# Optimization experiments

Hardware: AMD Instinct MI355X
Metric: run time of the kernel (lower is better)

Reference implementation:

```python
import jax, jax.numpy as jnp
import numpy as np

B, S, IN, H, OUT, L = 64, 2048, 208, 100, 98, 2


def setup_inputs() -> dict:
    key = jax.random.key(0)
    ks = jax.random.split(key, 11)
    sc = 1.0 / np.sqrt(H)  # pytorch GRU init scale
    return {
        "sequence": jax.random.normal(ks[0], (B, S, IN), jnp.float32),
        "h0": jnp.zeros((L, B, H), jnp.float32),
        "w_ih_l0": jax.random.normal(ks[1], (3 * H, IN), jnp.float32) * sc,
        "w_hh_l0": jax.random.normal(ks[2], (3 * H, H), jnp.float32) * sc,
        "b_ih_l0": jax.random.normal(ks[3], (3 * H,), jnp.float32) * sc,
        "b_hh_l0": jax.random.normal(ks[4], (3 * H,), jnp.float32) * sc,
        "w_ih_l1": jax.random.normal(ks[5], (3 * H, H), jnp.float32) * sc,
        "w_hh_l1": jax.random.normal(ks[6], (3 * H, H), jnp.float32) * sc,
        "b_ih_l1": jax.random.normal(ks[7], (3 * H,), jnp.float32) * sc,
        "b_hh_l1": jax.random.normal(ks[8], (3 * H,), jnp.float32) * sc,
        "w_out": jax.random.normal(ks[9], (OUT, H), jnp.float32) * sc,
        "b_out": jax.random.normal(ks[10], (OUT,), jnp.float32) * sc,
    }


def _gru_layer(x, h0, w_ih, w_hh, b_ih, b_hh):
    # x: (B,S,Din), h0: (B,H). PyTorch GRU gate order: r, z, n.
    Hd = h0.shape[-1]
    xg = jnp.einsum("bsi,gi->bsg", x, w_ih) + b_ih  # (B,S,3H) input projections, batched GEMM

    def step(h, xg_t):
        hg = h @ w_hh.T + b_hh  # (B,3H)
        xr, xz, xn = xg_t[:, :Hd], xg_t[:, Hd:2 * Hd], xg_t[:, 2 * Hd:]
        hr, hz, hn = hg[:, :Hd], hg[:, Hd:2 * Hd], hg[:, 2 * Hd:]
        r = jax.nn.sigmoid(xr + hr)
        z = jax.nn.sigmoid(xz + hz)
        n = jnp.tanh(xn + r * hn)
        h_new = (1.0 - z) * n + z * h
        return h_new, h_new

    h_last, ys = jax.lax.scan(step, h0, jnp.swapaxes(xg, 0, 1))  # scan over time
    return jnp.swapaxes(ys, 0, 1), h_last  # (B,S,H)


def reference(sequence, h0, w_ih_l0, w_hh_l0, b_ih_l0, b_hh_l0,
              w_ih_l1, w_hh_l1, b_ih_l1, b_hh_l1, w_out, b_out):
    # 2-layer unidirectional GRU (eval mode: inter-layer dropout inactive) + linear head
    y0, _ = _gru_layer(sequence, h0[0], w_ih_l0, w_hh_l0, b_ih_l0, b_hh_l0)
    y1, _ = _gru_layer(y0, h0[1], w_ih_l1, w_hh_l1, b_ih_l1, b_hh_l1)
    return jnp.einsum("bsh,oh->bso", y1, w_out) + b_out  # (B,S,OUT)
```

## Files before the change

kernel.cpp:

```cpp
#include <hip/hip_runtime.h>
#include <hip/hip_bf16.h>


#define GB_BM 64
#define GB_BN 64
#define GB_BK 16

__global__ __launch_bounds__(256)
void gemm_bias(const float* __restrict__ A, const float* __restrict__ W,
               const float* __restrict__ bias, float* __restrict__ C,
               int Sc, long a_bs, long a_ss, long c_bs, long c_ss,
               int N, int K)
{
    __shared__ float As[GB_BK][68];
    __shared__ float Bs[GB_BK][68];
    const int tid = threadIdx.x;
    const int m0 = blockIdx.x * GB_BM;
    const int n0 = blockIdx.y * GB_BN;

    const int lm = tid >> 2;
    const int lk = (tid & 3) << 2;
    const int row = m0 + lm;
    const float* arow = A + (long)(row / Sc) * a_bs + (long)(row % Sc) * a_ss;
    const int wrow = n0 + lm;
    const float* wrp = W + (long)wrow * K;
    const bool wv_ok = (wrow < N);

    const int tx = tid & 15;
    const int ty = tid >> 4;

    float acc[4][4] = {};

    for (int k0 = 0; k0 < K; k0 += GB_BK) {
        float4 av, bv;
        if (k0 + GB_BK <= K) {
            av = *(const float4*)(arow + k0 + lk);
            bv = wv_ok ? *(const float4*)(wrp + k0 + lk) : make_float4(0.f,0.f,0.f,0.f);
        } else {
            av = make_float4(0.f,0.f,0.f,0.f);
            bv = make_float4(0.f,0.f,0.f,0.f);
            const int kb = k0 + lk;
            if (kb + 0 < K) { av.x = arow[kb+0]; if (wv_ok) bv.x = wrp[kb+0]; }
            if (kb + 1 < K) { av.y = arow[kb+1]; if (wv_ok) bv.y = wrp[kb+1]; }
            if (kb + 2 < K) { av.z = arow[kb+2]; if (wv_ok) bv.z = wrp[kb+2]; }
            if (kb + 3 < K) { av.w = arow[kb+3]; if (wv_ok) bv.w = wrp[kb+3]; }
        }
        As[lk+0][lm] = av.x; As[lk+1][lm] = av.y; As[lk+2][lm] = av.z; As[lk+3][lm] = av.w;
        Bs[lk+0][lm] = bv.x; Bs[lk+1][lm] = bv.y; Bs[lk+2][lm] = bv.z; Bs[lk+3][lm] = bv.w;
        __syncthreads();
        #pragma unroll
        for (int kk = 0; kk < GB_BK; kk++) {
            float4 a  = *(const float4*)&As[kk][ty << 2];
            float4 bb = *(const float4*)&Bs[kk][tx << 2];
            float ar[4] = {a.x, a.y, a.z, a.w};
            float br[4] = {bb.x, bb.y, bb.z, bb.w};
            #pragma unroll
            for (int i = 0; i < 4; i++)
                #pragma unroll
                for (int j = 0; j < 4; j++)
                    acc[i][j] += ar[i] * br[j];
        }
        __syncthreads();
    }

    #pragma unroll
    for (int i = 0; i < 4; i++) {
        const int r = m0 + (ty << 2) + i;
        float* crow = C + (long)(r / Sc) * c_bs + (long)(r % Sc) * c_ss;
        #pragma unroll
        for (int j = 0; j < 4; j++) {
            const int col = n0 + (tx << 2) + j;
            if (col < N) crow[col] = acc[i][j] + bias[col];
        }
    }
}


__device__ __forceinline__ float fsig(float x)  { return 1.f / (1.f + __expf(-x)); }
__device__ __forceinline__ float ftanh(float x) { return 1.f - 2.f / (1.f + __expf(2.f * x)); }

__global__ __launch_bounds__(640, 1)
void gru_scan(const float* __restrict__ xg, const float* __restrict__ w_hh,
              const float* __restrict__ b_hh, const float* __restrict__ h_init,
              float* __restrict__ h_state, float* __restrict__ y,
              int Sc, int first)
{
    __shared__ __align__(16) float hs[100];
    __shared__ float hg_lds[300];
    __shared__ float xg_lds[300];

    const int tid = threadIdx.x;
    const int b = blockIdx.x;
    const int half = tid & 1;
    const int g = tid >> 1;
    const bool dot = (tid < 600);
    const bool even = dot && (half == 0);

    float4 wv[13];
    float bhh = 0.f;
    if (dot) {
        const float* wb = w_hh + g * 100 + half * 48;
        #pragma unroll
        for (int i = 0; i < 13; i++) wv[i] = *(const float4*)(wb + 4 * i);
        if (!half) wv[12] = make_float4(0.f, 0.f, 0.f, 0.f);
    }
    if (even) bhh = b_hh[g];

    float hcur = 0.f;
    if (tid < 100) {
        hcur = first ? h_init[b * 100 + tid] : h_state[b * 100 + tid];
        hs[tid] = hcur;
    }

    const float* xgb = xg + (size_t)b * Sc * 300;
    float xnext = 0.f;
    if (even) xnext = xgb[g];
    __syncthreads();

    for (int t = 0; t < Sc; t++) {
        const float xcur = xnext;
        if (even && (t + 1 < Sc)) xnext = xgb[(size_t)(t + 1) * 300 + g];

        float tot = 0.f;
        if (dot) {
            const float4* hs4 = (const float4*)hs;
            const int base = half * 12;
            float a0 = 0.f, a1 = 0.f;
            #pragma unroll
            for (int i = 0; i < 13; i++) {
                const float4 h4 = hs4[base + i];
                const float4 w = wv[i];
                a0 += w.x * h4.x; a1 += w.y * h4.y;
                a0 += w.z * h4.z; a1 += w.w * h4.w;
            }
            tot = a0 + a1;
            tot += __shfl_down(tot, 1);
        }
        if (even) { hg_lds[g] = tot + bhh; xg_lds[g] = xcur; }
        __syncthreads();

        if (tid < 100) {
            const float xr = xg_lds[tid], xz = xg_lds[100 + tid], xn = xg_lds[200 + tid];
            const float hr = hg_lds[tid], hz = hg_lds[100 + tid], hn = hg_lds[200 + tid];
            const float r = fsig(xr + hr);
            const float z = fsig(xz + hz);
            const float n = ftanh(xn + r * hn);
            hcur = (1.f - z) * n + z * hcur;
            hs[tid] = hcur;
            y[((size_t)b * Sc + t) * 100 + tid] = hcur;
        }
        __syncthreads();
    }

    if (tid < 100) h_state[b * 100 + tid] = hcur;
}


extern "C" void kernel_launch(void* const* d_in, const int* in_sizes, int n_in,
                              void* d_out, int out_size, void* d_ws, size_t ws_size,
                              hipStream_t stream)
{
    const float* seq    = (const float*)d_in[0];
    const float* h0     = (const float*)d_in[1];
    const float* w_ih0  = (const float*)d_in[2];
    const float* w_hh0  = (const float*)d_in[3];
    const float* b_ih0  = (const float*)d_in[4];
    const float* b_hh0  = (const float*)d_in[5];
    const float* w_ih1  = (const float*)d_in[6];
    const float* w_hh1  = (const float*)d_in[7];
    const float* b_ih1  = (const float*)d_in[8];
    const float* b_hh1  = (const float*)d_in[9];
    const float* w_out  = (const float*)d_in[10];
    const float* b_out  = (const float*)d_in[11];
    float* out = (float*)d_out;

    const int B = 64, S = 2048, IN = 208, H = 100, G = 300, OUT = 98;

    int Sc = S;
    while (Sc > 16) {
        size_t need = ((size_t)B * Sc * (G + H + H) + 2 * (size_t)B * H) * sizeof(float);
        if (need <= ws_size) break;
        Sc >>= 1;
    }
    const int NC = S / Sc;

    float* h0s = (float*)d_ws;
    float* h1s = h0s + (size_t)B * H;
    float* y0c = h1s + (size_t)B * H;
    float* y1c = y0c + (size_t)B * Sc * H;
    float* xgc = y1c + (size_t)B * Sc * H;

    const dim3 blk(256);
    const dim3 gX((B * Sc) / GB_BM, (G + GB_BN - 1) / GB_BN);
    const dim3 gO((B * Sc) / GB_BM, (OUT + GB_BN - 1) / GB_BN);

    for (int c = 0; c < NC; c++) {
        const int s0 = c * Sc;
        const int first = (c == 0);

        gemm_bias<<<gX, blk, 0, stream>>>(seq + (long)s0 * IN, w_ih0, b_ih0, xgc,
                                          Sc, (long)S * IN, (long)IN,
                                          (long)Sc * G, (long)G, G, IN);
        gru_scan<<<dim3(B), dim3(640), 0, stream>>>(xgc, w_hh0, b_hh0,
                                                    h0, h0s, y0c, Sc, first);
        gemm_bias<<<gX, blk, 0, stream>>>(y0c, w_ih1, b_ih1, xgc,
                                          Sc, (long)Sc * H, (long)H,
                                          (long)Sc * G, (long)G, G, H);
        gru_scan<<<dim3(B), dim3(640), 0, stream>>>(xgc, w_hh1, b_hh1,
                                                    h0 + (size_t)B * H, h1s, y1c, Sc, first);
        gemm_bias<<<gO, blk, 0, stream>>>(y1c, w_out, b_out, out + (long)s0 * OUT,
                                          Sc, (long)Sc * H, (long)H,
                                          (long)S * OUT, (long)OUT, OUT, H);
    }
}
```

Before: 3.054 ms.

## Fuse both GRU layers into one wavefront-pipelined scan kernel with fp16 dot2

Replaces the two per-layer scan kernels and the layer-1 input-projection GEMM with a single kernel. Layer 1 runs one step behind layer 0 inside the same time loop, and its input projection is computed on the fly from layer-0's hidden state. Recurrent weights are held in registers as packed fp16 and applied with fdot2, with hidden state broadcast via readlane instead of LDS reads. This removes a kernel launch, the y0 round trip and one recurrence pass, at the cost of fp16 precision in the recurrent dot products and a 1024-thread block.

Result: slower. 4.111 ms (+34.6%).

```diff
diff --git a/kernel.cpp b/kernel.cpp
--- a/kernel.cpp
+++ b/kernel.cpp
@@ -1,6 +1,136 @@
 #include <hip/hip_runtime.h>
 #include <hip/hip_bf16.h>
-
+#include <stdint.h>
+
+
+typedef __fp16 half2v __attribute__((ext_vector_type(2)));
+
+__device__ __forceinline__ float fsig(float x)  { return 1.f / (1.f + __expf(-x)); }
+__device__ __forceinline__ float ftanh(float x) { return 1.f - 2.f / (1.f + __expf(2.f * x)); }
+
+__device__ __forceinline__ uint32_t pkh2(float a, float b) {
+    half2v h = __builtin_amdgcn_cvt_pkrtz(a, b);
+    return __builtin_bit_cast(uint32_t, h);
+}
+
+__device__ __forceinline__ float dot2acc(uint32_t w, uint32_t h, float acc) {
+#if __has_builtin(__builtin_amdgcn_fdot2)
+    return __builtin_amdgcn_fdot2(__builtin_bit_cast(half2v, w),
+                                  __builtin_bit_cast(half2v, h), acc, false);
+#else
+    half2v wv = __builtin_bit_cast(half2v, w), hv = __builtin_bit_cast(half2v, h);
+    return acc + (float)wv.x * (float)hv.x + (float)wv.y * (float)hv.y;
+#endif
+}
+
+__device__ __forceinline__ void gru4(float4& h, float4 xr, float4 xz, float4 xn,
+                                     float4 hr, float4 hz, float4 hn) {
+    float r, z, n;
+    r = fsig(xr.x + hr.x); z = fsig(xz.x + hz.x); n = ftanh(xn.x + r * hn.x); h.x = (1.f - z) * n + z * h.x;
+    r = fsig(xr.y + hr.y); z = fsig(xz.y + hz.y); n = ftanh(xn.y + r * hn.y); h.y = (1.f - z) * n + z * h.y;
+    r = fsig(xr.z + hr.z); z = fsig(xz.z + hz.z); n = ftanh(xn.z + r * hn.z); h.z = (1.f - z) * n + z * h.z;
+    r = fsig(xr.w + hr.w); z = fsig(xz.w + hz.w); n = ftanh(xn.w + r * hn.w); h.w = (1.f - z) * n + z * h.w;
+}
+
+__global__ __launch_bounds__(1024, 4)
+void gru_fused(const float* __restrict__ xg0,
+               const float* __restrict__ w_hh0, const float* __restrict__ b_hh0,
+               const float* __restrict__ w_ih1, const float* __restrict__ b_ih1,
+               const float* __restrict__ w_hh1, const float* __restrict__ b_hh1,
+               const float* __restrict__ h_init,
+               float* __restrict__ h_state,
+               float* __restrict__ y1,
+               int Sc, int first)
+{
+    __shared__ __align__(16) float res[960];
+    __shared__ uint32_t hs0p[64];
+    __shared__ uint32_t hs1p[64];
+
+    const int tid = threadIdx.x, b = blockIdx.x;
+    const int lane = tid & 63;
+    const bool is_upd = (tid >= 960);
+
+    const float* wrow = w_hh0;
+    float bias = 0.f;
+    bool store_ok = false;
+    if (tid < 300)                    { wrow = w_hh0 + tid * 100;         bias = b_hh0[tid];       store_ok = true; }
+    else if (tid < 600)               { wrow = w_ih1 + (tid - 300) * 100; bias = b_ih1[tid - 300]; store_ok = true; }
+    else if (tid >= 640 && tid < 940) { wrow = w_hh1 + (tid - 640) * 100; bias = b_hh1[tid - 640]; store_ok = true; }
+
+    uint32_t w[50];
+    #pragma unroll
+    for (int i = 0; i < 25; i++) {
+        float4 v = ((const float4*)wrow)[i];
+        w[2 * i]     = pkh2(v.x, v.y);
+        w[2 * i + 1] = pkh2(v.z, v.w);
+    }
+    const uint32_t* hsrc = (tid < 640) ? hs0p : hs1p;
+
+    int role = -1, qi = 0;
+    if (is_upd) {
+        if (lane < 25)                    { role = 0; qi = lane; }
+        else if (lane >= 32 && lane < 57) { role = 1; qi = lane - 32; }
+    }
+    float4 h = make_float4(0.f, 0.f, 0.f, 0.f);
+    if (role >= 0) {
+        const float* hsg = (first ? h_init : h_state) + role * 6400 + b * 100;
+        h = ((const float4*)hsg)[qi];
+        uint32_t* hp = (role == 0) ? hs0p : hs1p;
+        hp[2 * qi]     = pkh2(h.x, h.y);
+        hp[2 * qi + 1] = pkh2(h.z, h.w);
+    }
+    const float* xrow_base = xg0 + (size_t)b * Sc * 300;
+    float4 c0, c1, c2, n0, n1, n2;
+    if (role == 0) {
+        c0 = ((const float4*)xrow_base)[qi];
+        c1 = ((const float4*)xrow_base)[25 + qi];
+        c2 = ((const float4*)xrow_base)[50 + qi];
+    }
+    __syncthreads();
+
+    for (int t = 0; t <= Sc; t++) {
+        if (!is_upd) {
+            uint32_t hp = hsrc[lane];
+            float a0 = bias, a1 = 0.f;
+            #pragma unroll
+            for (int k = 0; k < 50; k += 2) {
+                uint32_t h0b = (uint32_t)__builtin_amdgcn_readlane((int)hp, k);
+                a0 = dot2acc(w[k], h0b, a0);
+                uint32_t h1b = (uint32_t)__builtin_amdgcn_readlane((int)hp, k + 1);
+                a1 = dot2acc(w[k + 1], h1b, a1);
+            }
+            if (store_ok) res[tid] = a0 + a1;
+        } else if (role == 0) {
+            const float* nr = xrow_base + (size_t)min(t + 1, Sc - 1) * 300;
+            n0 = ((const float4*)nr)[qi];
+            n1 = ((const float4*)nr)[25 + qi];
+            n2 = ((const float4*)nr)[50 + qi];
+        }
+        __syncthreads();
+
+        if (role == 0 && t < Sc) {
+            const float4* r4 = (const float4*)res;
+            float4 hr = r4[qi], hz = r4[25 + qi], hn = r4[50 + qi];
+            gru4(h, c0, c1, c2, hr, hz, hn);
+            hs0p[2 * qi]     = pkh2(h.x, h.y);
+            hs0p[2 * qi + 1] = pkh2(h.z, h.w);
+            c0 = n0; c1 = n1; c2 = n2;
+        }
+        if (role == 1 && t >= 1) {
+            const float4* r4 = (const float4*)res;
+            float4 xr = r4[75 + qi],  xz = r4[100 + qi], xn = r4[125 + qi];
+            float4 hr = r4[160 + qi], hz = r4[185 + qi], hn = r4[210 + qi];
+            gru4(h, xr, xz, xn, hr, hz, hn);
+            hs1p[2 * qi]     = pkh2(h.x, h.y);
+            hs1p[2 * qi + 1] = pkh2(h.z, h.w);
+            ((float4*)(y1 + ((size_t)b * Sc + (t - 1)) * 100))[qi] = h;
+        }
+        __syncthreads();
+    }
+
+    if (role >= 0)
+        ((float4*)(h_state + role * 6400 + b * 100))[qi] = h;
+}
 
 #define GB_BM 64
 #define GB_BN 64
@@ -73,86 +203,6 @@
             if (col < N) crow[col] = acc[i][j] + bias[col];
         }
     }
-}
-
-
-__device__ __forceinline__ float fsig(float x)  { return 1.f / (1.f + __expf(-x)); }
-__device__ __forceinline__ float ftanh(float x) { return 1.f - 2.f / (1.f + __expf(2.f * x)); }
-
-__global__ __launch_bounds__(640, 1)
-void gru_scan(const float* __restrict__ xg, const float* __restrict__ w_hh,
-              const float* __restrict__ b_hh, const float* __restrict__ h_init,
-              float* __restrict__ h_state, float* __restrict__ y,
-              int Sc, int first)
-{
-    __shared__ __align__(16) float hs[100];
-    __shared__ float hg_lds[300];
-    __shared__ float xg_lds[300];
-
-    const int tid = threadIdx.x;
-    const int b = blockIdx.x;
-    const int half = tid & 1;
-    const int g = tid >> 1;
-    const bool dot = (tid < 600);
-    const bool even = dot && (half == 0);
-
-    float4 wv[13];
-    float bhh = 0.f;
-    if (dot) {
-        const float* wb = w_hh + g * 100 + half * 48;
-        #pragma unroll
-        for (int i = 0; i < 13; i++) wv[i] = *(const float4*)(wb + 4 * i);
-        if (!half) wv[12] = make_float4(0.f, 0.f, 0.f, 0.f);
-    }
-    if (even) bhh = b_hh[g];
-
-    float hcur = 0.f;
-    if (tid < 100) {
-        hcur = first ? h_init[b * 100 + tid] : h_state[b * 100 + tid];
-        hs[tid] = hcur;
-    }
-
-    const float* xgb = xg + (size_t)b * Sc * 300;
-    float xnext = 0.f;
-    if (even) xnext = xgb[g];
-    __syncthreads();
-
-    for (int t = 0; t < Sc; t++) {
-        const float xcur = xnext;
-        if (even && (t + 1 < Sc)) xnext = xgb[(size_t)(t + 1) * 300 + g];
-
-        float tot = 0.f;
-        if (dot) {
-            const float4* hs4 = (const float4*)hs;
-            const int base = half * 12;
-            float a0 = 0.f, a1 = 0.f;
-            #pragma unroll
-            for (int i = 0; i < 13; i++) {
-                const float4 h4 = hs4[base + i];
-                const float4 w = wv[i];
-                a0 += w.x * h4.x; a1 += w.y * h4.y;
-                a0 += w.z * h4.z; a1 += w.w * h4.w;
-            }
-            tot = a0 + a1;
-            tot += __shfl_down(tot, 1);
-        }
-        if (even) { hg_lds[g] = tot + bhh; xg_lds[g] = xcur; }
-        __syncthreads();
-
-        if (tid < 100) {
-            const float xr = xg_lds[tid], xz = xg_lds[100 + tid], xn = xg_lds[200 + tid];
-            const float hr = hg_lds[tid], hz = hg_lds[100 + tid], hn = hg_lds[200 + tid];
-            const float r = fsig(xr + hr);
-            const float z = fsig(xz + hz);
-            const float n = ftanh(xn + r * hn);
-            hcur = (1.f - z) * n + z * hcur;
-            hs[tid] = hcur;
-            y[((size_t)b * Sc + t) * 100 + tid] = hcur;
-        }
-        __syncthreads();
-    }
-
-    if (tid < 100) h_state[b * 100 + tid] = hcur;
 }
 
 
@@ -178,17 +228,15 @@
 
     int Sc = S;
     while (Sc > 16) {
-        size_t need = ((size_t)B * Sc * (G + H + H) + 2 * (size_t)B * H) * sizeof(float);
+        size_t need = ((size_t)B * Sc * (G + H) + 2 * (size_t)B * H) * sizeof(float);
         if (need <= ws_size) break;
         Sc >>= 1;
     }
     const int NC = S / Sc;
 
-    float* h0s = (float*)d_ws;
-    float* h1s = h0s + (size_t)B * H;
-    float* y0c = h1s + (size_t)B * H;
-    float* y1c = y0c + (size_t)B * Sc * H;
-    float* xgc = y1c + (size_t)B * Sc * H;
+    float* h_state = (float*)d_ws;
+    float* y1c     = h_state + 2 * (size_t)B * H;
+    float* xgc     = y1c + (size_t)B * Sc * H;
 
     const dim3 blk(256);
     const dim3 gX((B * Sc) / GB_BM, (G + GB_BN - 1) / GB_BN);
@@ -201,13 +249,10 @@
         gemm_bias<<<gX, blk, 0, stream>>>(seq + (long)s0 * IN, w_ih0, b_ih0, xgc,
                                           Sc, (long)S * IN, (long)IN,
                                           (long)Sc * G, (long)G, G, IN);
-        gru_scan<<<dim3(B), dim3(640), 0, stream>>>(xgc, w_hh0, b_hh0,
-                                                    h0, h0s, y0c, Sc, first);
-        gemm_bias<<<gX, blk, 0, stream>>>(y0c, w_ih1, b_ih1, xgc,
-                                          Sc, (long)Sc * H, (long)H,
-                                          (long)Sc * G, (long)G, G, H);
-        gru_scan<<<dim3(B), dim3(640), 0, stream>>>(xgc, w_hh1, b_hh1,
-                                                    h0 + (size_t)B * H, h1s, y1c, Sc, first);
+        gru_fused<<<dim3(B), dim3(1024), 0, stream>>>(xgc,
+                                                      w_hh0, b_hh0, w_ih1, b_ih1,
+                                                      w_hh1, b_hh1,
+                                                      h0, h_state, y1c, Sc, first);
         gemm_bias<<<gO, blk, 0, stream>>>(y1c, w_out, b_out, out + (long)s0 * OUT,
                                           Sc, (long)Sc * H, (long)H,
                                           (long)S * OUT, (long)OUT, OUT, H);
```
